# Kernel tuning notes

Hardware: AMD Instinct MI355X
Metric: run time of the kernel (lower is better)

The kernel has to match this reference:

```python
import jax, jax.numpy as jnp
import numpy as np


def setup_inputs() -> dict:
    key = jax.random.key(0)
    ks = jax.random.split(key, 8)
    N, D, G, H = 131072, 128, 2048, 512
    features = jax.random.normal(ks[0], (N, D), dtype=jnp.float32)
    graph_index = jnp.sort(jax.random.randint(ks[1], (N,), 0, G))
    s1 = 1.0 / np.sqrt(D)
    W_m = jax.random.uniform(ks[2], (H, D), jnp.float32, -s1, s1)
    b_m = jax.random.uniform(ks[3], (H,), jnp.float32, -s1, s1)
    s2 = 1.0 / np.sqrt(H)
    W_ih = jax.random.uniform(ks[4], (4 * H, 2 * H), jnp.float32, -s2, s2)
    W_hh = jax.random.uniform(ks[5], (4 * H, H), jnp.float32, -s2, s2)
    b_ih = jax.random.uniform(ks[6], (4 * H,), jnp.float32, -s2, s2)
    b_hh = jax.random.uniform(ks[7], (4 * H,), jnp.float32, -s2, s2)
    return dict(features=features, graph_index=graph_index, W_m=W_m, b_m=b_m,
                W_ih=W_ih, W_hh=W_hh, b_ih=b_ih, b_hh=b_hh, num_graphs=G)


def reference(features, graph_index, W_m, b_m, W_ih, W_hh, b_ih, b_hh, num_graphs):
    H = W_m.shape[0]
    LOOP = 3
    EPS = 1e-7
    NEG_BIG = -1e10
    m = features @ W_m.T + b_m                      # [N, H]
    h = jnp.zeros((num_graphs, H), m.dtype)
    c = jnp.zeros((num_graphs, H), m.dtype)
    q_star = jnp.zeros((num_graphs, 2 * H), m.dtype)
    for _ in range(LOOP):
        # PyTorch LSTMCell: gates in (i, f, g, o) order
        gates = q_star @ W_ih.T + h @ W_hh.T + (b_ih + b_hh)   # [G, 4H]
        i_g, f_g, g_g, o_g = jnp.split(gates, 4, axis=-1)
        c = jax.nn.sigmoid(f_g) * c + jax.nn.sigmoid(i_g) * jnp.tanh(g_g)
        h = jax.nn.sigmoid(o_g) * jnp.tanh(c)
        # attention scores per node against its graph's query h
        e = jnp.sum(m * h[graph_index], axis=-1, keepdims=True)  # [N, 1]
        e_max = jax.ops.segment_max(e, graph_index, num_segments=num_graphs)
        e_max = jax.lax.stop_gradient(
            jnp.where(jnp.isfinite(e_max), e_max, NEG_BIG))
        e = e - e_max[graph_index]
        exp_e = jnp.exp(jnp.clip(e, -30.0, 20.0))
        exp_sum = jax.ops.segment_sum(exp_e, graph_index, num_segments=num_graphs)
        a = exp_e / (exp_sum[graph_index] + EPS)                 # [N, 1]
        r = jax.ops.segment_sum(m * a, graph_index, num_segments=num_graphs)  # [G, H]
        q_star = jnp.concatenate([h, r], axis=-1)                # [G, 2H]
    return q_star
```

## Files before the change

### kernel.cpp

```cpp
#include <hip/hip_runtime.h>

#define N_NODES 131072
#define DIM     128
#define NG      2048
#define HD      512

typedef unsigned short u16;
typedef _Float16 half8 __attribute__((ext_vector_type(8)));
typedef float  f32x4  __attribute__((ext_vector_type(4)));

__device__ u16   g_fb[(size_t)N_NODES * DIM];
__device__ u16   g_wm[(size_t)HD * DIM];
__device__ u16   g_wmT[(size_t)DIM * HD];
__device__ u16   g_wgf[(size_t)2048 * 640];
__device__ u16   g_wih2[(size_t)2048 * 512];
__device__ float g_bc[2048];
__device__ float g_bf[2048];
__device__ float g_gh[2048];
__device__ float g_h0[512];
__device__ float g_c0[512];
__device__ float g_w20[128];
__device__ float g_tp[NG];
__device__ u16   g_Acat[(size_t)NG * 640];
__device__ float g_c[(size_t)NG * HD];
__device__ int   g_start[NG + 1];
__device__ int   g_isbf16;
__device__ int   g_idx64;

__device__ __forceinline__ float bf2f(u16 u) {
  unsigned v = ((unsigned)u) << 16;
  float f; __builtin_memcpy(&f, &v, 4); return f;
}
__device__ __forceinline__ float u2f_hi(unsigned u) {
  unsigned v = u & 0xFFFF0000u;
  float f; __builtin_memcpy(&f, &v, 4); return f;
}
__device__ __forceinline__ float u2f_lo(unsigned u) {
  unsigned v = u << 16;
  float f; __builtin_memcpy(&f, &v, 4); return f;
}
__device__ __forceinline__ u16 f2bf(float f) {
  unsigned u; __builtin_memcpy(&u, &f, 4);
  u += 0x7FFFu + ((u >> 16) & 1u);
  return (u16)(u >> 16);
}
__device__ __forceinline__ u16 f2h(float f) {
  _Float16 h = (_Float16)f; u16 u; __builtin_memcpy(&u, &h, 2); return u;
}
__device__ __forceinline__ float h2f(u16 u) {
  _Float16 h; __builtin_memcpy(&h, &u, 2); return (float)h;
}
__device__ __forceinline__ float rdf(const void* p, int i) {
  return g_isbf16 ? bf2f(((const u16*)p)[i]) : ((const float*)p)[i];
}

#define GLD16(gp, lp) __builtin_amdgcn_global_load_lds(                          \
    (const __attribute__((address_space(1))) void*)(gp),                         \
    (__attribute__((address_space(3))) void*)(lp), 16, 0, 0)

__global__ void k_detect(const void* feat, const void* gi) {
  __shared__ int cnt;
  if (threadIdx.x == 0) cnt = 0;
  __syncthreads();
  u16 u = ((const u16*)feat)[threadIdx.x];
  float v = bf2f(u);
  float a = fabsf(v);
  int ok = (v == v) && a >= 1e-6f && a <= 1e6f;
  atomicAdd(&cnt, ok);
  __syncthreads();
  if (threadIdx.x == 0) {
    g_isbf16 = (cnt >= 230);
    g_idx64 = (((const int*)gi)[N_NODES - 1] == 0);
  }
}

#define NFP ((size_t)N_NODES * DIM / 2)
#define NWP ((size_t)HD * DIM / 2)
#define NWT ((size_t)DIM * HD / 2)
#define NW1 ((size_t)2048 * 512 / 2)
#define NW2 ((size_t)2048 * 512 / 2)
#define FB_BLOCKS 1024
#define W_PAIRS (NWP + NWT + NW1 + NW2)
#define W_BLOCKS ((int)((W_PAIRS + 255) / 256))
__global__ __launch_bounds__(256) void k_cvt_all(const void* f, const void* wm,
                                                 const void* wih, const void* whh) {
  const int isb = g_isbf16;
  const int b = blockIdx.x, t = threadIdx.x;
  if (b < FB_BLOCKS) {
    if (isb) return;
    for (size_t p = (size_t)b * 256 + t; p < NFP; p += (size_t)FB_BLOCKS * 256) {
      float2 v = ((const float2*)f)[p];
      ((unsigned*)g_fb)[p] = (unsigned)f2h(v.x) | ((unsigned)f2h(v.y) << 16);
    }
    return;
  }
  size_t i = (size_t)(b - FB_BLOCKS) * 256 + t;
  if (i < NWP) {
    float v0, v1;
    if (isb) {
      unsigned pr = ((const unsigned*)wm)[i];
      v0 = bf2f((u16)pr); v1 = bf2f((u16)(pr >> 16));
    } else {
      float2 v = ((const float2*)wm)[i];
      v0 = v.x; v1 = v.y;
    }
    ((unsigned*)g_wm)[i] = (unsigned)f2h(v0) | ((unsigned)f2h(v1) << 16);
  } else if (i < NWP + NWT) {
    size_t p = i - NWP;
    int d = (int)(p >> 8), j = (int)(p & 255) * 2;
    float v0 = rdf(wm, j * DIM + d);
    float v1 = rdf(wm, (j + 1) * DIM + d);
    ((unsigned*)g_wmT)[(size_t)d * 256 + (j >> 1)] =
        (unsigned)f2h(v0) | ((unsigned)f2h(v1) << 16);
  } else if (i < NWP + NWT + NW1) {
    size_t p = i - NWP - NWT;
    int n = (int)(p >> 8), kp = (int)(p & 255), k = kp * 2;
    int orig = (n & 3) * 512 + (n >> 2);
    float v0 = rdf(wih, orig * 1024 + k)     + rdf(whh, orig * 512 + k);
    float v1 = rdf(wih, orig * 1024 + k + 1) + rdf(whh, orig * 512 + k + 1);
    ((unsigned*)g_wgf)[(size_t)n * 320 + kp] =
        (unsigned)f2h(v0) | ((unsigned)f2h(v1) << 16);
  } else if (i < NWP + NWT + NW1 + NW2) {
    size_t p = i - NWP - NWT - NW1;
    int n = (int)(p >> 8), kp = (int)(p & 255), k = kp * 2;
    int orig = (n & 3) * 512 + (n >> 2);
    float v0 = rdf(wih, orig * 1024 + 512 + k);
    float v1 = rdf(wih, orig * 1024 + 512 + k + 1);
    ((unsigned*)g_wih2)[(size_t)n * 256 + kp] =
        (unsigned)f2h(v0) | ((unsigned)f2h(v1) << 16);
  }
}

__global__ __launch_bounds__(256) void k_misc1(const void* giv,
                                               const void* b_ih, const void* b_hh) {
  const int t = threadIdx.x;
  if (blockIdx.x < 512) {
    int n = blockIdx.x * 256 + t;
    const int idx64 = g_idx64;
    int g = idx64 ? (int)((const long long*)giv)[n] : ((const int*)giv)[n];
    if (n == 0) {
      for (int x = 0; x <= g; ++x) g_start[x] = 0;
    } else {
      int gp = idx64 ? (int)((const long long*)giv)[n - 1] : ((const int*)giv)[n - 1];
      for (int x = gp + 1; x <= g; ++x) g_start[x] = n;
    }
    if (n == N_NODES - 1) {
      for (int x = g + 1; x <= NG; ++x) g_start[x] = N_NODES;
    }
    return;
  }
  __shared__ float s_h[512];
  __shared__ float s_red[4][128];
  for (int j = t; j < 512; j += 256) {
    float xi = rdf(b_ih, j)        + rdf(b_hh, j);
    float xg = rdf(b_ih, j + 1024) + rdf(b_hh, j + 1024);
    float xo = rdf(b_ih, j + 1536) + rdf(b_hh, j + 1536);
    float si = 1.f / (1.f + __expf(-xi));
    float tg = tanhf(xg);
    float so = 1.f / (1.f + __expf(-xo));
    float cn = si * tg;
    float hn = so * tanhf(cn);
    g_c0[j] = cn;
    g_h0[j] = hn;
    s_h[j] = hn;
  }
  __syncthreads();
  const int dg = t & 15, jg = t >> 4;
  float a8[8] = {};
  for (int jj = 0; jj < 32; ++jj) {
    const int j = jg * 32 + jj;
    half8 wv = *(const half8*)(g_wm + (size_t)j * 128 + dg * 8);
    const float hv = s_h[j];
#pragma unroll
    for (int d = 0; d < 8; ++d) a8[d] += hv * (float)wv[d];
  }
#pragma unroll
  for (int d = 0; d < 8; ++d) {
    a8[d] += __shfl_xor(a8[d], 16, 64);
    a8[d] += __shfl_xor(a8[d], 32, 64);
  }
  const int w = t >> 6;
  if ((t & 63) < 16) {
    *(f32x4*)&s_red[w][dg * 8]     = *(f32x4*)&a8[0];
    *(f32x4*)&s_red[w][dg * 8 + 4] = *(f32x4*)&a8[4];
  }
  __syncthreads();
  if (t < 128)
    g_w20[t] = s_red[0][t] + s_red[1][t] + s_red[2][t] + s_red[3][t];
}

__global__ __launch_bounds__(256) void k_misc2(const void* b_ih, const void* b_hh,
                                               const void* b_m) {
  const int t = threadIdx.x;
  if (blockIdx.x < 128) {
    __shared__ float s_bm[512], s_h0[512];
    for (int p = t; p < 512; p += 256) {
      s_bm[p] = rdf(b_m, p);
      s_h0[p] = g_h0[p];
    }
    __syncthreads();
    const int rloc = t >> 4, k = t & 15;
    const int n = blockIdx.x * 16 + rloc;
    float sbf = 0.f, sgh = 0.f;
#pragma unroll
    for (int j = 0; j < 4; ++j) {
      const int e = k * 8 + j * 128;
      half8 w2v = *(const half8*)(g_wih2 + (size_t)n * 512 + e);
      half8 w1v = *(const half8*)(g_wgf  + (size_t)n * 640 + e);
#pragma unroll
      for (int d = 0; d < 8; ++d) {
        sbf += (float)w2v[d] * s_bm[e + d];
        sgh += (float)w1v[d] * s_h0[e + d];
      }
    }
#pragma unroll
    for (int o = 1; o < 16; o <<= 1) {
      sbf += __shfl_xor(sbf, o, 64);
      sgh += __shfl_xor(sgh, o, 64);
    }
    if (k == 0) {
      const int orig = (n & 3) * 512 + (n >> 2);
      g_bf[n] = sbf;
      g_gh[n] = sgh;
      g_bc[n] = rdf(b_ih, orig) + rdf(b_hh, orig);
    }
    return;
  }
  __shared__ u16 As[64 * 64];
  __shared__ u16 Bs[64 * 64];
  const int bx = blockIdx.x - 128;
  const int lid = t & 63, w = t >> 6;
  const int m0 = (bx & 31) * 64, n0 = (bx >> 5) * 64;
  const int rr = lid & 15, quad = lid >> 4;
  const int rsub = lid >> 3;
  const int cs = (lid & 7) ^ rsub;
  const int wm = (w >> 1) * 32, wn = (w & 1) * 32;
  f32x4 acc[2][2] = {};
  for (int kt = 0; kt < 8; ++kt) {
    const int k0 = kt * 64;
    GLD16(g_wih2 + (size_t)(m0 + w * 16 + rsub) * 512 + k0 + cs * 8, As + (w * 16) * 64);
    GLD16(g_wih2 + (size_t)(m0 + w * 16 + 8 + rsub) * 512 + k0 + cs * 8, As + (w * 16 + 8) * 64);
    GLD16(g_wmT + (size_t)(n0 + w * 16 + rsub) * 512 + k0 + cs * 8, Bs + (w * 16) * 64);
    GLD16(g_wmT + (size_t)(n0 + w * 16 + 8 + rsub) * 512 + k0 + cs * 8, Bs + (w * 16 + 8) * 64);
    __syncthreads();
#pragma unroll
    for (int kk = 0; kk < 2; ++kk) {
      const int qb = kk * 4 + quad;
      const int sw = (qb ^ (rr & 7)) << 3;
      half8 af[2], bfr[2];
#pragma unroll
      for (int i = 0; i < 2; ++i) af[i]  = *(const half8*)(As + (wm + i * 16 + rr) * 64 + sw);
#pragma unroll
      for (int j = 0; j < 2; ++j) bfr[j] = *(const half8*)(Bs + (wn + j * 16 + rr) * 64 + sw);
#pragma unroll
      for (int i = 0; i < 2; ++i)
#pragma unroll
        for (int j = 0; j < 2; ++j)
          acc[i][j] = __builtin_amdgcn_mfma_f32_16x16x32_f16(bfr[j], af[i], acc[i][j], 0, 0, 0);
    }
    __syncthreads();
  }
#pragma unroll
  for (int i = 0; i < 2; ++i)
#pragma unroll
    for (int j = 0; j < 2; ++j) {
      const int row = m0 + wm + i * 16 + rr;
      const int c0 = n0 + wn + j * 16 + quad * 4;
      u16 h4[4];
#pragma unroll
      for (int r = 0; r < 4; ++r) h4[r] = f2h(acc[i][j][r]);
      *(uint2*)(g_wgf + (size_t)row * 640 + 512 + c0) =
          make_uint2((unsigned)h4[0] | ((unsigned)h4[1] << 16),
                     (unsigned)h4[2] | ((unsigned)h4[3] << 16));
    }
}

__global__ __launch_bounds__(256) void k_gemm_fused(int ktiles2, int aoff,
                                                    int useGh, int first,
                                                    int wout,
                                                    void* __restrict__ out) {
  __shared__ u16 As[2][64 * 64];
  __shared__ u16 Bs[2][64 * 64];
  const int t = threadIdx.x, lid = t & 63, w = t >> 6;
  const int m0 = blockIdx.x * 64, n0 = blockIdx.y * 64;
  const int rr = lid & 15, quad = lid >> 4;
  const int rsub = lid >> 3;
  const int cs = (lid & 7) ^ rsub;
  const int wm = (w >> 1) * 32, wn = (w & 1) * 32;
  f32x4 acc[2][2] = {};
  for (int kt2 = 0; kt2 < ktiles2; ++kt2) {
#pragma unroll
    for (int b = 0; b < 2; ++b) {
      const int k0 = aoff + (kt2 * 2 + b) * 64;
      GLD16(g_Acat + (size_t)(m0 + w * 16 + rsub) * 640 + k0 + cs * 8, As[b] + (w * 16) * 64);
      GLD16(g_Acat + (size_t)(m0 + w * 16 + 8 + rsub) * 640 + k0 + cs * 8, As[b] + (w * 16 + 8) * 64);
      GLD16(g_wgf  + (size_t)(n0 + w * 16 + rsub) * 640 + k0 + cs * 8, Bs[b] + (w * 16) * 64);
      GLD16(g_wgf  + (size_t)(n0 + w * 16 + 8 + rsub) * 640 + k0 + cs * 8, Bs[b] + (w * 16 + 8) * 64);
    }
    __syncthreads();
#pragma unroll
    for (int b = 0; b < 2; ++b)
#pragma unroll
      for (int kk = 0; kk < 2; ++kk) {
        const int qb = kk * 4 + quad;
        const int sw = (qb ^ (rr & 7)) << 3;
        half8 af[2], bfr[2];
#pragma unroll
        for (int i = 0; i < 2; ++i) af[i]  = *(const half8*)(As[b] + (wm + i * 16 + rr) * 64 + sw);
#pragma unroll
        for (int j = 0; j < 2; ++j) bfr[j] = *(const half8*)(Bs[b] + (wn + j * 16 + rr) * 64 + sw);
#pragma unroll
        for (int i = 0; i < 2; ++i)
#pragma unroll
          for (int j = 0; j < 2; ++j)
            acc[i][j] = __builtin_amdgcn_mfma_f32_16x16x32_f16(bfr[j], af[i], acc[i][j], 0, 0, 0);
      }
    __syncthreads();
  }
  const int isb = g_isbf16;
#pragma unroll
  for (int i = 0; i < 2; ++i) {
    const int row = m0 + wm + i * 16 + rr;
    const float tp = g_tp[row];
#pragma unroll
    for (int j = 0; j < 2; ++j) {
      const int c0 = n0 + wn + j * 16 + quad * 4;
      const int jj = c0 >> 2;
      float4 bc = *(const float4*)(g_bc + c0);
      float4 bf = *(const float4*)(g_bf + c0);
      float gx = 0.f, gy = 0.f, gz = 0.f, gw = 0.f;
      if (useGh) {
        float4 gh = *(const float4*)(g_gh + c0);
        gx = gh.x; gy = gh.y; gz = gh.z; gw = gh.w;
      }
      float xi = acc[i][j][0] + bc.x + gx + tp * bf.x;
      float xf = acc[i][j][1] + bc.y + gy + tp * bf.y;
      float xg = acc[i][j][2] + bc.z + gz + tp * bf.z;
      float xo = acc[i][j][3] + bc.w + gw + tp * bf.w;
      float si = 1.f / (1.f + __expf(-xi));
      float sf = 1.f / (1.f + __expf(-xf));
      float tg = tanhf(xg);
      float so = 1.f / (1.f + __expf(-xo));
      float cp = first ? g_c0[jj] : g_c[(size_t)row * 512 + jj];
      float cn = sf * cp + si * tg;
      float hn = so * tanhf(cn);
      g_c[(size_t)row * 512 + jj] = cn;
      g_Acat[(size_t)row * 640 + jj] = f2h(hn);
      if (wout) {
        if (isb) ((u16*)out)[(size_t)row * 1024 + jj] = f2bf(hn);
        else     ((float*)out)[(size_t)row * 1024 + jj] = hn;
      }
    }
  }
}

__global__ __launch_bounds__(256) void k_attn_s(const void* __restrict__ feat,
                                                int mode) {
  const int g = blockIdx.x;
  const int t = threadIdx.x, lid = t & 63, wid = t >> 6;
  const int c = lid & 15;
  const int slot = lid >> 4;
  __shared__ float s_m[4], s_l[4];
  __shared__ float s_s[4][DIM];
  __shared__ float s_h[512];
  const int s = g_start[g], e = g_start[g + 1];
  const int israw = g_isbf16;
  float w2r[8];
  if (mode) {
    for (int p = t; p < 512; p += 256)
      s_h[p] = h2f(g_Acat[(size_t)g * 640 + p]);
    __syncthreads();
    const int jg = t >> 4;
    float a8[8] = {};
    for (int jj = 0; jj < 32; ++jj) {
      const int j = jg * 32 + jj;
      half8 wv = *(const half8*)(g_wm + (size_t)j * 128 + c * 8);
      const float hv = s_h[j];
#pragma unroll
      for (int d = 0; d < 8; ++d) a8[d] += hv * (float)wv[d];
    }
#pragma unroll
    for (int d = 0; d < 8; ++d) {
      a8[d] += __shfl_xor(a8[d], 16, 64);
      a8[d] += __shfl_xor(a8[d], 32, 64);
    }
    if (lid < 16) {
      *(f32x4*)&s_s[wid][c * 8]     = *(f32x4*)&a8[0];
      *(f32x4*)&s_s[wid][c * 8 + 4] = *(f32x4*)&a8[4];
    }
    __syncthreads();
#pragma unroll
    for (int d = 0; d < 8; ++d)
      w2r[d] = s_s[0][c * 8 + d] + s_s[1][c * 8 + d] +
               s_s[2][c * 8 + d] + s_s[3][c * 8 + d];
  } else {
    *(float4*)(w2r)     = *(const float4*)(g_w20 + c * 8);
    *(float4*)(w2r + 4) = *(const float4*)(g_w20 + c * 8 + 4);
  }
  float mrun = -3.0e38f, lsum = 0.f;
  float racc[8] = {0.f, 0.f, 0.f, 0.f, 0.f, 0.f, 0.f, 0.f};
  for (int nb = s + wid * 4; nb < e; nb += 16) {
    const int n = nb + slot;
    float fv[8], d;
    if (n < e) {
      if (israw) {
        uint4 q = *(const uint4*)((const u16*)feat + (size_t)n * DIM + c * 8);
        fv[0] = u2f_lo(q.x); fv[1] = u2f_hi(q.x);
        fv[2] = u2f_lo(q.y); fv[3] = u2f_hi(q.y);
        fv[4] = u2f_lo(q.z); fv[5] = u2f_hi(q.z);
        fv[6] = u2f_lo(q.w); fv[7] = u2f_hi(q.w);
      } else {
        half8 hv = *(const half8*)(g_fb + (size_t)n * DIM + c * 8);
#pragma unroll
        for (int j = 0; j < 8; ++j) fv[j] = (float)hv[j];
      }
      d = 0.f;
#pragma unroll
      for (int j = 0; j < 8; ++j) d += fv[j] * w2r[j];
    } else {
      d = -1.0e30f;
#pragma unroll
      for (int j = 0; j < 8; ++j) fv[j] = 0.f;
    }
#pragma unroll
    for (int o = 1; o < 16; o <<= 1) d += __shfl_xor(d, o, 64);
    float m4 = fmaxf(d, __shfl_xor(d, 16, 64));
    m4 = fmaxf(m4, __shfl_xor(m4, 32, 64));
    float mnew = fmaxf(mrun, m4);
    float sc = __expf(mrun - mnew);
    float w = __expf(d - mnew);
    lsum = lsum * sc + w;
#pragma unroll
    for (int j = 0; j < 8; ++j) racc[j] = racc[j] * sc + w * fv[j];
    mrun = mnew;
  }
  float lt = lsum + __shfl_xor(lsum, 16, 64);
  lt += __shfl_xor(lt, 32, 64);
#pragma unroll
  for (int j = 0; j < 8; ++j) {
    racc[j] += __shfl_xor(racc[j], 16, 64);
    racc[j] += __shfl_xor(racc[j], 32, 64);
  }
  if (lid == 0) s_m[wid] = mrun;
  __syncthreads();
  float gmax = fmaxf(fmaxf(s_m[0], s_m[1]), fmaxf(s_m[2], s_m[3]));
  float scw = __expf(mrun - gmax);
  if (lid < 16) {
    float4 lo = make_float4(racc[0] * scw, racc[1] * scw, racc[2] * scw, racc[3] * scw);
    float4 hi = make_float4(racc[4] * scw, racc[5] * scw, racc[6] * scw, racc[7] * scw);
    *(float4*)&s_s[wid][c * 8] = lo;
    *(float4*)&s_s[wid][c * 8 + 4] = hi;
  }
  if (lid == 0) s_l[wid] = lt * scw;
  __syncthreads();
  float total = s_l[0] + s_l[1] + s_l[2] + s_l[3];
  float inv = 1.f / (total + 1e-7f);
  if (t == 0) g_tp[g] = total * inv;
  if (t < 64) {
    int d0 = t * 2;
    float v0 = (s_s[0][d0] + s_s[1][d0] + s_s[2][d0] + s_s[3][d0]) * inv;
    float v1 = (s_s[0][d0 + 1] + s_s[1][d0 + 1] + s_s[2][d0 + 1] + s_s[3][d0 + 1]) * inv;
    ((unsigned*)g_Acat)[(size_t)g * 320 + 256 + t] =
        (unsigned)f2h(v0) | ((unsigned)f2h(v1) << 16);
  }
}

__global__ __launch_bounds__(256) void k_r(const void* __restrict__ bias,
                                           void* __restrict__ out) {
  __shared__ u16 As[64 * 64];
  __shared__ u16 Bs[64 * 64];
  const int t = threadIdx.x, lid = t & 63, w = t >> 6;
  const int m0 = blockIdx.x * 64, n0 = blockIdx.y * 64;
  const int rr = lid & 15, quad = lid >> 4;
  const int rsub = lid >> 3;
  const int cs = (lid & 7) ^ rsub;
  const int wm = (w >> 1) * 32, wn = (w & 1) * 32;
  f32x4 acc[2][2] = {};
  for (int kt = 0; kt < 2; ++kt) {
    const int k0 = kt * 64;
    GLD16(g_Acat + (size_t)(m0 + w * 16 + rsub) * 640 + 512 + k0 + cs * 8, As + (w * 16) * 64);
    GLD16(g_Acat + (size_t)(m0 + w * 16 + 8 + rsub) * 640 + 512 + k0 + cs * 8, As + (w * 16 + 8) * 64);
    GLD16(g_wm + (size_t)(n0 + w * 16 + rsub) * 128 + k0 + cs * 8, Bs + (w * 16) * 64);
    GLD16(g_wm + (size_t)(n0 + w * 16 + 8 + rsub) * 128 + k0 + cs * 8, Bs + (w * 16 + 8) * 64);
    __syncthreads();
#pragma unroll
    for (int kk = 0; kk < 2; ++kk) {
      const int qb = kk * 4 + quad;
      const int sw = (qb ^ (rr & 7)) << 3;
      half8 af[2], bfr[2];
#pragma unroll
      for (int i = 0; i < 2; ++i) af[i]  = *(const half8*)(As + (wm + i * 16 + rr) * 64 + sw);
#pragma unroll
      for (int j = 0; j < 2; ++j) bfr[j] = *(const half8*)(Bs + (wn + j * 16 + rr) * 64 + sw);
#pragma unroll
      for (int i = 0; i < 2; ++i)
#pragma unroll
        for (int j = 0; j < 2; ++j)
          acc[i][j] = __builtin_amdgcn_mfma_f32_16x16x32_f16(bfr[j], af[i], acc[i][j], 0, 0, 0);
    }
    __syncthreads();
  }
  const int isb = g_isbf16;
#pragma unroll
  for (int i = 0; i < 2; ++i) {
    const int row = m0 + wm + i * 16 + rr;
    const float tp = g_tp[row];
#pragma unroll
    for (int j = 0; j < 2; ++j) {
      const int c0 = n0 + wn + j * 16 + quad * 4;
      float rv[4];
#pragma unroll
      for (int r = 0; r < 4; ++r) rv[r] = acc[i][j][r] + tp * rdf(bias, c0 + r);
      if (isb) {
        u16 b4[4];
#pragma unroll
        for (int r = 0; r < 4; ++r) b4[r] = f2bf(rv[r]);
        *(uint2*)((u16*)out + (size_t)row * 1024 + 512 + c0) =
            make_uint2((unsigned)b4[0] | ((unsigned)b4[1] << 16),
                       (unsigned)b4[2] | ((unsigned)b4[3] << 16));
      } else {
        *(f32x4*)((float*)out + (size_t)row * 1024 + 512 + c0) = *(f32x4*)rv;
      }
    }
  }
}

extern "C" void kernel_launch(void* const* d_in, const int* in_sizes, int n_in,
                              void* d_out, int out_size, void* d_ws, size_t ws_size,
                              hipStream_t stream) {
  const void* features = d_in[0];
  const void* gidx     = d_in[1];
  const void* W_m      = d_in[2];
  const void* b_m      = d_in[3];
  const void* W_ih     = d_in[4];
  const void* W_hh     = d_in[5];
  const void* b_ih     = d_in[6];
  const void* b_hh     = d_in[7];

  k_detect<<<1, 256, 0, stream>>>(features, gidx);
  k_cvt_all<<<FB_BLOCKS + W_BLOCKS, 256, 0, stream>>>(features, W_m, W_ih, W_hh);
  k_misc1<<<513, 256, 0, stream>>>(gidx, b_ih, b_hh);
  k_misc2<<<192, 256, 0, stream>>>(b_ih, b_hh, b_m);
  k_attn_s<<<NG, 256, 0, stream>>>(features, 0);
  k_gemm_fused<<<dim3(32, 32), 256, 0, stream>>>(1, 512, 1, 1, 0, d_out);
  k_attn_s<<<NG, 256, 0, stream>>>(features, 1);
  k_gemm_fused<<<dim3(32, 32), 256, 0, stream>>>(5, 0, 0, 0, 1, d_out);
  k_attn_s<<<NG, 256, 0, stream>>>(features, 1);
  k_r<<<dim3(32, 8), 256, 0, stream>>>(b_m, d_out);
}
```

Before: 240.7 us.

## Drop fp16 feature conversion, merge setup kernels, fuse final projection into attention

Removes the full fp16 copy of the node features, so the fp32 attention path reads the raw features directly instead of paying an extra conversion pass. Merges the weight-conversion and segment-start kernels into one grid-stride kernel, and folds the h0/w20 setup and the bias GEMM into a single kernel. The last r-projection GEMM is fused into the final attention kernel as a per-graph matvec against W_m, and the last LSTM h goes to a separate buffer so it can run. The trade-off is higher feature read bandwidth in fp32 mode and a less efficient scalar matvec in place of the MFMA GEMM.

```diff
diff --git a/kernel.cpp b/kernel.cpp
--- a/kernel.cpp
+++ b/kernel.cpp
@@ -9,7 +9,6 @@
 typedef _Float16 half8 __attribute__((ext_vector_type(8)));
 typedef float  f32x4  __attribute__((ext_vector_type(4)));
 
-__device__ u16   g_fb[(size_t)N_NODES * DIM];
 __device__ u16   g_wm[(size_t)HD * DIM];
 __device__ u16   g_wmT[(size_t)DIM * HD];
 __device__ u16   g_wgf[(size_t)2048 * 640];
@@ -17,11 +16,11 @@
 __device__ float g_bc[2048];
 __device__ float g_bf[2048];
 __device__ float g_gh[2048];
-__device__ float g_h0[512];
 __device__ float g_c0[512];
 __device__ float g_w20[128];
 __device__ float g_tp[NG];
 __device__ u16   g_Acat[(size_t)NG * 640];
+__device__ u16   g_h3[(size_t)NG * HD];
 __device__ float g_c[(size_t)NG * HD];
 __device__ int   g_start[NG + 1];
 __device__ int   g_isbf16;
@@ -74,133 +73,88 @@
   }
 }
 
-#define NFP ((size_t)N_NODES * DIM / 2)
 #define NWP ((size_t)HD * DIM / 2)
 #define NWT ((size_t)DIM * HD / 2)
 #define NW1 ((size_t)2048 * 512 / 2)
 #define NW2 ((size_t)2048 * 512 / 2)
-#define FB_BLOCKS 1024
 #define W_PAIRS (NWP + NWT + NW1 + NW2)
-#define W_BLOCKS ((int)((W_PAIRS + 255) / 256))
-__global__ __launch_bounds__(256) void k_cvt_all(const void* f, const void* wm,
-                                                 const void* wih, const void* whh) {
-  const int isb = g_isbf16;
-  const int b = blockIdx.x, t = threadIdx.x;
-  if (b < FB_BLOCKS) {
-    if (isb) return;
-    for (size_t p = (size_t)b * 256 + t; p < NFP; p += (size_t)FB_BLOCKS * 256) {
-      float2 v = ((const float2*)f)[p];
-      ((unsigned*)g_fb)[p] = (unsigned)f2h(v.x) | ((unsigned)f2h(v.y) << 16);
-    }
-    return;
-  }
-  size_t i = (size_t)(b - FB_BLOCKS) * 256 + t;
-  if (i < NWP) {
-    float v0, v1;
-    if (isb) {
-      unsigned pr = ((const unsigned*)wm)[i];
-      v0 = bf2f((u16)pr); v1 = bf2f((u16)(pr >> 16));
+
+__global__ __launch_bounds__(256) void k_s0(const void* gidxv, const void* wmp,
+                                            const void* wih, const void* whh) {
+  const int t = threadIdx.x;
+  for (size_t i = (size_t)blockIdx.x * 256 + t; i < W_PAIRS;
+       i += (size_t)gridDim.x * 256) {
+    if (i < NWP) {
+      float v0, v1;
+      if (g_isbf16) {
+        unsigned pr = ((const unsigned*)wmp)[i];
+        v0 = bf2f((u16)pr); v1 = bf2f((u16)(pr >> 16));
+      } else {
+        float2 v = ((const float2*)wmp)[i];
+        v0 = v.x; v1 = v.y;
+      }
+      ((unsigned*)g_wm)[i] = (unsigned)f2h(v0) | ((unsigned)f2h(v1) << 16);
+    } else if (i < NWP + NWT) {
+      size_t p = i - NWP;
+      int d = (int)(p >> 8), j = (int)(p & 255) * 2;
+      float v0 = rdf(wmp, j * DIM + d);
+      float v1 = rdf(wmp, (j + 1) * DIM + d);
+      ((unsigned*)g_wmT)[(size_t)d * 256 + (j >> 1)] =
+          (unsigned)f2h(v0) | ((unsigned)f2h(v1) << 16);
+    } else if (i < NWP + NWT + NW1) {
+      size_t p = i - NWP - NWT;
+      int n = (int)(p >> 8), kp = (int)(p & 255), k = kp * 2;
+      int orig = (n & 3) * 512 + (n >> 2);
+      float v0 = rdf(wih, orig * 1024 + k)     + rdf(whh, orig * 512 + k);
+      float v1 = rdf(wih, orig * 1024 + k + 1) + rdf(whh, orig * 512 + k + 1);
+      ((unsigned*)g_wgf)[(size_t)n * 320 + kp] =
+          (unsigned)f2h(v0) | ((unsigned)f2h(v1) << 16);
     } else {
-      float2 v = ((const float2*)wm)[i];
-      v0 = v.x; v1 = v.y;
-    }
-    ((unsigned*)g_wm)[i] = (unsigned)f2h(v0) | ((unsigned)f2h(v1) << 16);
-  } else if (i < NWP + NWT) {
-    size_t p = i - NWP;
-    int d = (int)(p >> 8), j = (int)(p & 255) * 2;
-    float v0 = rdf(wm, j * DIM + d);
-    float v1 = rdf(wm, (j + 1) * DIM + d);
-    ((unsigned*)g_wmT)[(size_t)d * 256 + (j >> 1)] =
-        (unsigned)f2h(v0) | ((unsigned)f2h(v1) << 16);
-  } else if (i < NWP + NWT + NW1) {
-    size_t p = i - NWP - NWT;
-    int n = (int)(p >> 8), kp = (int)(p & 255), k = kp * 2;
-    int orig = (n & 3) * 512 + (n >> 2);
-    float v0 = rdf(wih, orig * 1024 + k)     + rdf(whh, orig * 512 + k);
-    float v1 = rdf(wih, orig * 1024 + k + 1) + rdf(whh, orig * 512 + k + 1);
-    ((unsigned*)g_wgf)[(size_t)n * 320 + kp] =
-        (unsigned)f2h(v0) | ((unsigned)f2h(v1) << 16);
-  } else if (i < NWP + NWT + NW1 + NW2) {
-    size_t p = i - NWP - NWT - NW1;
-    int n = (int)(p >> 8), kp = (int)(p & 255), k = kp * 2;
-    int orig = (n & 3) * 512 + (n >> 2);
-    float v0 = rdf(wih, orig * 1024 + 512 + k);
-    float v1 = rdf(wih, orig * 1024 + 512 + k + 1);
-    ((unsigned*)g_wih2)[(size_t)n * 256 + kp] =
-        (unsigned)f2h(v0) | ((unsigned)f2h(v1) << 16);
-  }
-}
-
-__global__ __launch_bounds__(256) void k_misc1(const void* giv,
-                                               const void* b_ih, const void* b_hh) {
-  const int t = threadIdx.x;
+      size_t p = i - NWP - NWT - NW1;
+      int n = (int)(p >> 8), kp = (int)(p & 255), k = kp * 2;
+      int orig = (n & 3) * 512 + (n >> 2);
+      float v0 = rdf(wih, orig * 1024 + 512 + k);
+      float v1 = rdf(wih, orig * 1024 + 512 + k + 1);
+      ((unsigned*)g_wih2)[(size_t)n * 256 + kp] =
+          (unsigned)f2h(v0) | ((unsigned)f2h(v1) << 16);
+    }
+  }
   if (blockIdx.x < 512) {
     int n = blockIdx.x * 256 + t;
     const int idx64 = g_idx64;
-    int g = idx64 ? (int)((const long long*)giv)[n] : ((const int*)giv)[n];
+    int gg = idx64 ? (int)((const long long*)gidxv)[n] : ((const int*)gidxv)[n];
     if (n == 0) {
-      for (int x = 0; x <= g; ++x) g_start[x] = 0;
+      for (int x = 0; x <= gg; ++x) g_start[x] = 0;
     } else {
-      int gp = idx64 ? (int)((const long long*)giv)[n - 1] : ((const int*)giv)[n - 1];
-      for (int x = gp + 1; x <= g; ++x) g_start[x] = n;
+      int gp = idx64 ? (int)((const long long*)gidxv)[n - 1] : ((const int*)gidxv)[n - 1];
+      for (int x = gp + 1; x <= gg; ++x) g_start[x] = n;
     }
     if (n == N_NODES - 1) {
-      for (int x = g + 1; x <= NG; ++x) g_start[x] = N_NODES;
-    }
-    return;
-  }
-  __shared__ float s_h[512];
-  __shared__ float s_red[4][128];
-  for (int j = t; j < 512; j += 256) {
-    float xi = rdf(b_ih, j)        + rdf(b_hh, j);
-    float xg = rdf(b_ih, j + 1024) + rdf(b_hh, j + 1024);
-    float xo = rdf(b_ih, j + 1536) + rdf(b_hh, j + 1536);
-    float si = 1.f / (1.f + __expf(-xi));
-    float tg = tanhf(xg);
-    float so = 1.f / (1.f + __expf(-xo));
-    float cn = si * tg;
-    float hn = so * tanhf(cn);
-    g_c0[j] = cn;
-    g_h0[j] = hn;
-    s_h[j] = hn;
-  }
-  __syncthreads();
-  const int dg = t & 15, jg = t >> 4;
-  float a8[8] = {};
-  for (int jj = 0; jj < 32; ++jj) {
-    const int j = jg * 32 + jj;
-    half8 wv = *(const half8*)(g_wm + (size_t)j * 128 + dg * 8);
-    const float hv = s_h[j];
-#pragma unroll
-    for (int d = 0; d < 8; ++d) a8[d] += hv * (float)wv[d];
-  }
-#pragma unroll
-  for (int d = 0; d < 8; ++d) {
-    a8[d] += __shfl_xor(a8[d], 16, 64);
-    a8[d] += __shfl_xor(a8[d], 32, 64);
-  }
-  const int w = t >> 6;
-  if ((t & 63) < 16) {
-    *(f32x4*)&s_red[w][dg * 8]     = *(f32x4*)&a8[0];
-    *(f32x4*)&s_red[w][dg * 8 + 4] = *(f32x4*)&a8[4];
-  }
-  __syncthreads();
-  if (t < 128)
-    g_w20[t] = s_red[0][t] + s_red[1][t] + s_red[2][t] + s_red[3][t];
-}
-
-__global__ __launch_bounds__(256) void k_misc2(const void* b_ih, const void* b_hh,
-                                               const void* b_m) {
-  const int t = threadIdx.x;
-  if (blockIdx.x < 128) {
-    __shared__ float s_bm[512], s_h0[512];
+      for (int x = gg + 1; x <= NG; ++x) g_start[x] = N_NODES;
+    }
+  }
+}
+
+__global__ __launch_bounds__(256) void k_s1(const void* bih, const void* bhh,
+                                            const void* bm) {
+  alignas(16) __shared__ char smem[16384];
+  const int t = threadIdx.x, b = blockIdx.x;
+  if (b < 128) {
+    float* s_bm = (float*)smem;
+    float* s_h0 = s_bm + 512;
     for (int p = t; p < 512; p += 256) {
-      s_bm[p] = rdf(b_m, p);
-      s_h0[p] = g_h0[p];
+      s_bm[p] = rdf(bm, p);
+      float xi = rdf(bih, p)        + rdf(bhh, p);
+      float xg = rdf(bih, p + 1024) + rdf(bhh, p + 1024);
+      float xo = rdf(bih, p + 1536) + rdf(bhh, p + 1536);
+      float si = 1.f / (1.f + __expf(-xi));
+      float tg = tanhf(xg);
+      float so = 1.f / (1.f + __expf(-xo));
+      s_h0[p] = so * tanhf(si * tg);
     }
     __syncthreads();
     const int rloc = t >> 4, k = t & 15;
-    const int n = blockIdx.x * 16 + rloc;
+    const int n = b * 16 + rloc;
     float sbf = 0.f, sgh = 0.f;
 #pragma unroll
     for (int j = 0; j < 4; ++j) {
@@ -222,71 +176,109 @@
       const int orig = (n & 3) * 512 + (n >> 2);
       g_bf[n] = sbf;
       g_gh[n] = sgh;
-      g_bc[n] = rdf(b_ih, orig) + rdf(b_hh, orig);
-    }
-    return;
-  }
-  __shared__ u16 As[64 * 64];
-  __shared__ u16 Bs[64 * 64];
-  const int bx = blockIdx.x - 128;
-  const int lid = t & 63, w = t >> 6;
-  const int m0 = (bx & 31) * 64, n0 = (bx >> 5) * 64;
+      g_bc[n] = rdf(bih, orig) + rdf(bhh, orig);
+    }
+  } else if (b < 192) {
+    u16* As = (u16*)smem;
+    u16* Bs = As + 4096;
+    const int bx = b - 128;
+    const int lid = t & 63, w = t >> 6;
+    const int m0 = (bx & 31) * 64, n0 = (bx >> 5) * 64;
+    const int rr = lid & 15, quad = lid >> 4;
+    const int rsub = lid >> 3;
+    const int cs = (lid & 7) ^ rsub;
+    const int wm = (w >> 1) * 32, wn = (w & 1) * 32;
+    f32x4 acc[2][2] = {};
+    for (int kt = 0; kt < 8; ++kt) {
+      const int k0 = kt * 64;
+      GLD16(g_wih2 + (size_t)(m0 + w * 16 + rsub) * 512 + k0 + cs * 8, As + (w * 16) * 64);
+      GLD16(g_wih2 + (size_t)(m0 + w * 16 + 8 + rsub) * 512 + k0 + cs * 8, As + (w * 16 + 8) * 64);
+      GLD16(g_wmT + (size_t)(n0 + w * 16 + rsub) * 512 + k0 + cs * 8, Bs + (w * 16) * 64);
+      GLD16(g_wmT + (size_t)(n0 + w * 16 + 8 + rsub) * 512 + k0 + cs * 8, Bs + (w * 16 + 8) * 64);
+      __syncthreads();
+#pragma unroll
+      for (int kk = 0; kk < 2; ++kk) {
+        const int qb = kk * 4 + quad;
+        const int sw = (qb ^ (rr & 7)) << 3;
+        half8 af[2], bfr[2];
+#pragma unroll
+        for (int i = 0; i < 2; ++i) af[i]  = *(const half8*)(As + (wm + i * 16 + rr) * 64 + sw);
+#pragma unroll
+        for (int j = 0; j < 2; ++j) bfr[j] = *(const half8*)(Bs + (wn + j * 16 + rr) * 64 + sw);
+#pragma unroll
+        for (int i = 0; i < 2; ++i)
+#pragma unroll
+          for (int j = 0; j < 2; ++j)
+            acc[i][j] = __builtin_amdgcn_mfma_f32_16x16x32_f16(bfr[j], af[i], acc[i][j], 0, 0, 0);
+      }
+      __syncthreads();
+    }
+#pragma unroll
+    for (int i = 0; i < 2; ++i)
+#pragma unroll
+      for (int j = 0; j < 2; ++j) {
+        const int row = m0 + wm + i * 16 + rr;
+        const int c0 = n0 + wn + j * 16 + quad * 4;
+        u16 h4[4];
+#pragma unroll
+        for (int r = 0; r < 4; ++r) h4[r] = f2h(acc[i][j][r]);
+        *(uint2*)(g_wgf + (size_t)row * 640 + 512 + c0) =
+            make_uint2((unsigned)h4[0] | ((unsigned)h4[1] << 16),
+                       (unsigned)h4[2] | ((unsigned)h4[3] << 16));
+      }
+  } else if (b == 192) {
+    float* s_h   = (float*)smem;
+    float* s_red = s_h + 512;
+    for (int j = t; j < 512; j += 256) {
+      float xi = rdf(bih, j)        + rdf(bhh, j);
+      float xg = rdf(bih, j + 1024) + rdf(bhh, j + 1024);
+      float xo = rdf(bih, j + 1536) + rdf(bhh, j + 1536);
+      float si = 1.f / (1.f + __expf(-xi));
+      float tg = tanhf(xg);
+      float so = 1.f / (1.f + __expf(-xo));
+      float cn = si * tg;
+      float hn = so * tanhf(cn);
+      g_c0[j] = cn;
+      s_h[j] = hn;
+    }
+    __syncthreads();
+    const int dg = t & 15, jg = t >> 4;
+    float a8[8] = {};
+    for (int jj = 0; jj < 32; ++jj) {
+      const int j = jg * 32 + jj;
+      half8 wv = *(const half8*)(g_wm + (size_t)j * 128 + dg * 8);
+      const float hv = s_h[j];
+#pragma unroll
+      for (int d = 0; d < 8; ++d) a8[d] += hv * (float)wv[d];
+    }
+#pragma unroll
+    for (int d = 0; d < 8; ++d) {
+      a8[d] += __shfl_xor(a8[d], 16, 64);
+      a8[d] += __shfl_xor(a8[d], 32, 64);
+    }
+    const int w = t >> 6;
+    if ((t & 63) < 16) {
+      *(f32x4*)&s_red[w * 128 + dg * 8]     = *(f32x4*)&a8[0];
+      *(f32x4*)&s_red[w * 128 + dg * 8 + 4] = *(f32x4*)&a8[4];
+    }
+    __syncthreads();
+    if (t < 128)
+      g_w20[t] = s_red[t] + s_red[128 + t] + s_red[256 + t] + s_red[384 + t];
+  }
+}
+
+__global__ __launch_bounds__(256) void k_gemm(int ktiles2, int aoff, int useGh,
+                                              int first, int wout, int h3out,
+                                              void* __restrict__ out) {
+  alignas(16) __shared__ u16 As[2][64 * 64];
+  alignas(16) __shared__ u16 Bs[2][64 * 64];
+  const int t = threadIdx.x, lid = t & 63, w = t >> 6;
+  const int m0 = (blockIdx.x & 31) * 64, n0 = (blockIdx.x >> 5) * 64;
   const int rr = lid & 15, quad = lid >> 4;
   const int rsub = lid >> 3;
   const int cs = (lid & 7) ^ rsub;
   const int wm = (w >> 1) * 32, wn = (w & 1) * 32;
-  f32x4 acc[2][2] = {};
-  for (int kt = 0; kt < 8; ++kt) {
-    const int k0 = kt * 64;
-    GLD16(g_wih2 + (size_t)(m0 + w * 16 + rsub) * 512 + k0 + cs * 8, As + (w * 16) * 64);
-    GLD16(g_wih2 + (size_t)(m0 + w * 16 + 8 + rsub) * 512 + k0 + cs * 8, As + (w * 16 + 8) * 64);
-    GLD16(g_wmT + (size_t)(n0 + w * 16 + rsub) * 512 + k0 + cs * 8, Bs + (w * 16) * 64);
-    GLD16(g_wmT + (size_t)(n0 + w * 16 + 8 + rsub) * 512 + k0 + cs * 8, Bs + (w * 16 + 8) * 64);
-    __syncthreads();
-#pragma unroll
-    for (int kk = 0; kk < 2; ++kk) {
-      const int qb = kk * 4 + quad;
-      const int sw = (qb ^ (rr & 7)) << 3;
-      half8 af[2], bfr[2];
-#pragma unroll
-      for (int i = 0; i < 2; ++i) af[i]  = *(const half8*)(As + (wm + i * 16 + rr) * 64 + sw);
-#pragma unroll
-      for (int j = 0; j < 2; ++j) bfr[j] = *(const half8*)(Bs + (wn + j * 16 + rr) * 64 + sw);
-#pragma unroll
-      for (int i = 0; i < 2; ++i)
-#pragma unroll
-        for (int j = 0; j < 2; ++j)
-          acc[i][j] = __builtin_amdgcn_mfma_f32_16x16x32_f16(bfr[j], af[i], acc[i][j], 0, 0, 0);
-    }
-    __syncthreads();
-  }
-#pragma unroll
-  for (int i = 0; i < 2; ++i)
-#pragma unroll
-    for (int j = 0; j < 2; ++j) {
-      const int row = m0 + wm + i * 16 + rr;
-      const int c0 = n0 + wn + j * 16 + quad * 4;
-      u16 h4[4];
-#pragma unroll
-      for (int r = 0; r < 4; ++r) h4[r] = f2h(acc[i][j][r]);
-      *(uint2*)(g_wgf + (size_t)row * 640 + 512 + c0) =
-          make_uint2((unsigned)h4[0] | ((unsigned)h4[1] << 16),
-                     (unsigned)h4[2] | ((unsigned)h4[3] << 16));
-    }
-}
-
-__global__ __launch_bounds__(256) void k_gemm_fused(int ktiles2, int aoff,
-                                                    int useGh, int first,
-                                                    int wout,
-                                                    void* __restrict__ out) {
-  __shared__ u16 As[2][64 * 64];
-  __shared__ u16 Bs[2][64 * 64];
-  const int t = threadIdx.x, lid = t & 63, w = t >> 6;
-  const int m0 = blockIdx.x * 64, n0 = blockIdx.y * 64;
-  const int rr = lid & 15, quad = lid >> 4;
-  const int rsub = lid >> 3;
-  const int cs = (lid & 7) ^ rsub;
-  const int wm = (w >> 1) * 32, wn = (w & 1) * 32;
+  const int isb = g_isbf16;
   f32x4 acc[2][2] = {};
   for (int kt2 = 0; kt2 < ktiles2; ++kt2) {
 #pragma unroll
@@ -317,7 +309,6 @@
       }
     __syncthreads();
   }
-  const int isb = g_isbf16;
 #pragma unroll
   for (int i = 0; i < 2; ++i) {
     const int row = m0 + wm + i * 16 + rr;
@@ -345,7 +336,8 @@
       float cn = sf * cp + si * tg;
       float hn = so * tanhf(cn);
       g_c[(size_t)row * 512 + jj] = cn;
-      g_Acat[(size_t)row * 640 + jj] = f2h(hn);
+      if (h3out) g_h3[(size_t)row * 512 + jj] = f2h(hn);
+      else       g_Acat[(size_t)row * 640 + jj] = f2h(hn);
       if (wout) {
         if (isb) ((u16*)out)[(size_t)row * 1024 + jj] = f2bf(hn);
         else     ((float*)out)[(size_t)row * 1024 + jj] = hn;
@@ -354,21 +346,27 @@
   }
 }
 
-__global__ __launch_bounds__(256) void k_attn_s(const void* __restrict__ feat,
-                                                int mode) {
+__global__ __launch_bounds__(256) void k_attn(const void* __restrict__ feat, int mode,
+                                              int hsel, int fin,
+                                              void* __restrict__ out,
+                                              const void* __restrict__ bm) {
+  __shared__ float s_m[4], s_l[4];
+  __shared__ float s_s[4][DIM];
+  __shared__ float s_h[512];
+  __shared__ float s_keep[DIM];
+  __shared__ float s_tpv[1];
   const int g = blockIdx.x;
   const int t = threadIdx.x, lid = t & 63, wid = t >> 6;
   const int c = lid & 15;
   const int slot = lid >> 4;
-  __shared__ float s_m[4], s_l[4];
-  __shared__ float s_s[4][DIM];
-  __shared__ float s_h[512];
+  const int israw = g_isbf16;
   const int s = g_start[g], e = g_start[g + 1];
-  const int israw = g_isbf16;
   float w2r[8];
   if (mode) {
+    const u16* hsrc = hsel ? g_h3 : g_Acat;
+    const int hstr = hsel ? 512 : 640;
     for (int p = t; p < 512; p += 256)
-      s_h[p] = h2f(g_Acat[(size_t)g * 640 + p]);
+      s_h[p] = h2f(hsrc[(size_t)g * hstr + p]);
     __syncthreads();
     const int jg = t >> 4;
     float a8[8] = {};
@@ -393,6 +391,7 @@
     for (int d = 0; d < 8; ++d)
       w2r[d] = s_s[0][c * 8 + d] + s_s[1][c * 8 + d] +
                s_s[2][c * 8 + d] + s_s[3][c * 8 + d];
+    __syncthreads();
   } else {
     *(float4*)(w2r)     = *(const float4*)(g_w20 + c * 8);
     *(float4*)(w2r + 4) = *(const float4*)(g_w20 + c * 8 + 4);
@@ -410,9 +409,11 @@
         fv[4] = u2f_lo(q.z); fv[5] = u2f_hi(q.z);
         fv[6] = u2f_lo(q.w); fv[7] = u2f_hi(q.w);
       } else {
-        half8 hv = *(const half8*)(g_fb + (size_t)n * DIM + c * 8);
-#pragma unroll
-        for (int j = 0; j < 8; ++j) fv[j] = (float)hv[j];
+        const float* fp = (const float*)feat + (size_t)n * DIM + c * 8;
+        float4 f0 = *(const float4*)fp;
+        float4 f1 = *(const float4*)(fp + 4);
+        fv[0] = f0.x; fv[1] = f0.y; fv[2] = f0.z; fv[3] = f0.w;
+        fv[4] = f1.x; fv[5] = f1.y; fv[6] = f1.z; fv[7] = f1.w;
       }
       d = 0.f;
 #pragma unroll
@@ -448,79 +449,50 @@
   if (lid < 16) {
     float4 lo = make_float4(racc[0] * scw, racc[1] * scw, racc[2] * scw, racc[3] * scw);
     float4 hi = make_float4(racc[4] * scw, racc[5] * scw, racc[6] * scw, racc[7] * scw);
-    *(float4*)&s_s[wid][c * 8] = lo;
-    *(float4*)&s_s[wid][c * 8 + 4] = hi;
+    *(f32x4*)&s_s[wid][c * 8] = *(f32x4*)&lo;
+    *(f32x4*)&s_s[wid][c * 8 + 4] = *(f32x4*)&hi;
   }
   if (lid == 0) s_l[wid] = lt * scw;
   __syncthreads();
   float total = s_l[0] + s_l[1] + s_l[2] + s_l[3];
   float inv = 1.f / (total + 1e-7f);
-  if (t == 0) g_tp[g] = total * inv;
-  if (t < 64) {
-    int d0 = t * 2;
-    float v0 = (s_s[0][d0] + s_s[1][d0] + s_s[2][d0] + s_s[3][d0]) * inv;
-    float v1 = (s_s[0][d0 + 1] + s_s[1][d0 + 1] + s_s[2][d0 + 1] + s_s[3][d0 + 1]) * inv;
-    ((unsigned*)g_Acat)[(size_t)g * 320 + 256 + t] =
-        (unsigned)f2h(v0) | ((unsigned)f2h(v1) << 16);
-  }
-}
-
-__global__ __launch_bounds__(256) void k_r(const void* __restrict__ bias,
-                                           void* __restrict__ out) {
-  __shared__ u16 As[64 * 64];
-  __shared__ u16 Bs[64 * 64];
-  const int t = threadIdx.x, lid = t & 63, w = t >> 6;
-  const int m0 = blockIdx.x * 64, n0 = blockIdx.y * 64;
-  const int rr = lid & 15, quad = lid >> 4;
-  const int rsub = lid >> 3;
-  const int cs = (lid & 7) ^ rsub;
-  const int wm = (w >> 1) * 32, wn = (w & 1) * 32;
-  f32x4 acc[2][2] = {};
-  for (int kt = 0; kt < 2; ++kt) {
-    const int k0 = kt * 64;
-    GLD16(g_Acat + (size_t)(m0 + w * 16 + rsub) * 640 + 512 + k0 + cs * 8, As + (w * 16) * 64);
-    GLD16(g_Acat + (size_t)(m0 + w * 16 + 8 + rsub) * 640 + 512 + k0 + cs * 8, As + (w * 16 + 8) * 64);
-    GLD16(g_wm + (size_t)(n0 + w * 16 + rsub) * 128 + k0 + cs * 8, Bs + (w * 16) * 64);
-    GLD16(g_wm + (size_t)(n0 + w * 16 + 8 + rsub) * 128 + k0 + cs * 8, Bs + (w * 16 + 8) * 64);
-    __syncthreads();
-#pragma unroll
-    for (int kk = 0; kk < 2; ++kk) {
-      const int qb = kk * 4 + quad;
-      const int sw = (qb ^ (rr & 7)) << 3;
-      half8 af[2], bfr[2];
-#pragma unroll
-      for (int i = 0; i < 2; ++i) af[i]  = *(const half8*)(As + (wm + i * 16 + rr) * 64 + sw);
-#pragma unroll
-      for (int j = 0; j < 2; ++j) bfr[j] = *(const half8*)(Bs + (wn + j * 16 + rr) * 64 + sw);
-#pragma unroll
-      for (int i = 0; i < 2; ++i)
-#pragma unroll
-        for (int j = 0; j < 2; ++j)
-          acc[i][j] = __builtin_amdgcn_mfma_f32_16x16x32_f16(bfr[j], af[i], acc[i][j], 0, 0, 0);
-    }
-    __syncthreads();
-  }
-  const int isb = g_isbf16;
-#pragma unroll
-  for (int i = 0; i < 2; ++i) {
-    const int row = m0 + wm + i * 16 + rr;
-    const float tp = g_tp[row];
-#pragma unroll
-    for (int j = 0; j < 2; ++j) {
-      const int c0 = n0 + wn + j * 16 + quad * 4;
-      float rv[4];
-#pragma unroll
-      for (int r = 0; r < 4; ++r) rv[r] = acc[i][j][r] + tp * rdf(bias, c0 + r);
-      if (isb) {
-        u16 b4[4];
-#pragma unroll
-        for (int r = 0; r < 4; ++r) b4[r] = f2bf(rv[r]);
-        *(uint2*)((u16*)out + (size_t)row * 1024 + 512 + c0) =
-            make_uint2((unsigned)b4[0] | ((unsigned)b4[1] << 16),
-                       (unsigned)b4[2] | ((unsigned)b4[3] << 16));
-      } else {
-        *(f32x4*)((float*)out + (size_t)row * 1024 + 512 + c0) = *(f32x4*)rv;
-      }
+  if (!fin) {
+    if (t == 0) g_tp[g] = total * inv;
+    if (t < 64) {
+      int d0 = t * 2;
+      float v0 = (s_s[0][d0] + s_s[1][d0] + s_s[2][d0] + s_s[3][d0]) * inv;
+      float v1 = (s_s[0][d0 + 1] + s_s[1][d0 + 1] + s_s[2][d0 + 1] + s_s[3][d0 + 1]) * inv;
+      ((unsigned*)g_Acat)[(size_t)g * 320 + 256 + t] =
+          (unsigned)f2h(v0) | ((unsigned)f2h(v1) << 16);
+    }
+  } else {
+    if (t == 0) s_tpv[0] = total * inv;
+    if (t < 64) {
+      int d0 = t * 2;
+      s_keep[d0]     = (s_s[0][d0] + s_s[1][d0] + s_s[2][d0] + s_s[3][d0]) * inv;
+      s_keep[d0 + 1] = (s_s[0][d0 + 1] + s_s[1][d0 + 1] + s_s[2][d0 + 1] + s_s[3][d0 + 1]) * inv;
+    }
+    __syncthreads();
+    const int jj = t * 2;
+    float a0 = 0.f, a1 = 0.f;
+    for (int db = 0; db < 16; ++db) {
+      half8 w0 = *(const half8*)(g_wm + (size_t)jj * 128 + db * 8);
+      half8 w1 = *(const half8*)(g_wm + (size_t)(jj + 1) * 128 + db * 8);
+#pragma unroll
+      for (int d = 0; d < 8; ++d) {
+        float kv = s_keep[db * 8 + d];
+        a0 += kv * (float)w0[d];
+        a1 += kv * (float)w1[d];
+      }
+    }
+    float tp = s_tpv[0];
+    float r0 = a0 + tp * rdf(bm, jj);
+    float r1 = a1 + tp * rdf(bm, jj + 1);
+    if (israw) {
+      ((unsigned*)out)[((size_t)g * 1024 + 512 + jj) >> 1] =
+          (unsigned)f2bf(r0) | ((unsigned)f2bf(r1) << 16);
+    } else {
+      *(float2*)((float*)out + (size_t)g * 1024 + 512 + jj) = make_float2(r0, r1);
     }
   }
 }
@@ -538,13 +510,11 @@
   const void* b_hh     = d_in[7];
 
   k_detect<<<1, 256, 0, stream>>>(features, gidx);
-  k_cvt_all<<<FB_BLOCKS + W_BLOCKS, 256, 0, stream>>>(features, W_m, W_ih, W_hh);
-  k_misc1<<<513, 256, 0, stream>>>(gidx, b_ih, b_hh);
-  k_misc2<<<192, 256, 0, stream>>>(b_ih, b_hh, b_m);
-  k_attn_s<<<NG, 256, 0, stream>>>(features, 0);
-  k_gemm_fused<<<dim3(32, 32), 256, 0, stream>>>(1, 512, 1, 1, 0, d_out);
-  k_attn_s<<<NG, 256, 0, stream>>>(features, 1);
-  k_gemm_fused<<<dim3(32, 32), 256, 0, stream>>>(5, 0, 0, 0, 1, d_out);
-  k_attn_s<<<NG, 256, 0, stream>>>(features, 1);
-  k_r<<<dim3(32, 8), 256, 0, stream>>>(b_m, d_out);
-}
+  k_s0<<<1024, 256, 0, stream>>>(gidx, W_m, W_ih, W_hh);
+  k_s1<<<193, 256, 0, stream>>>(b_ih, b_hh, b_m);
+  k_attn<<<NG, 256, 0, stream>>>(features, 0, 0, 0, d_out, b_m);
+  k_gemm<<<1024, 256, 0, stream>>>(1, 512, 1, 1, 0, 0, d_out);
+  k_attn<<<NG, 256, 0, stream>>>(features, 1, 0, 0, d_out, b_m);
+  k_gemm<<<1024, 256, 0, stream>>>(5, 0, 0, 0, 1, 1, d_out);
+  k_attn<<<NG, 256, 0, stream>>>(features, 1, 1, 1, d_out, b_m);
+}
```

After: 362.4 us. +50.6%, slower.
